# Performance work log

Measured on AMD Instinct MI355X. Metric: run time of the kernel, lower is better.

## Reference

```python
import jax, jax.numpy as jnp
import numpy as np


def setup_inputs() -> dict:
    key = jax.random.key(0)
    k1, k2, k3, k4 = jax.random.split(key, 4)
    B, C, H, W = 8, 64, 64, 64
    K = C // 8
    x = jax.random.normal(k1, (B, C, H, W), dtype=jnp.float32)
    # 1x1 conv weights (no bias): stored as [out_ch, in_ch]
    Wf = jax.random.normal(k2, (K, C), dtype=jnp.float32) * 0.05
    Wg = jax.random.normal(k3, (K, C), dtype=jnp.float32) * 0.05
    Wh = jax.random.normal(k4, (C, C), dtype=jnp.float32) * 0.05
    # gamma initialized to zero in the module; use a nonzero value so the
    # attention path contributes to the output (and gradients) in testing.
    gamma = jnp.array([0.5], dtype=jnp.float32)
    return {"x": x, "Wf": Wf, "Wg": Wg, "Wh": Wh, "gamma": gamma}


def reference(x, Wf, Wg, Wh, gamma):
    B, C, H, W = x.shape
    N = H * W
    xf = x.reshape(B, C, N)                       # [B, C, N]
    f = jnp.einsum('kc,bcn->bkn', Wf, xf)         # [B, C//8, N]
    g = jnp.einsum('kc,bcn->bkn', Wg, xf)         # [B, C//8, N]
    h = jnp.einsum('oc,bcn->bon', Wh, xf)         # [B, C, N]
    # beta[b, i, j] = f[b,:,i] . g[b,:,j]  (unscaled attention logits)
    beta = jnp.einsum('bki,bkj->bij', f, g)       # [B, N, N]
    beta = jax.nn.softmax(beta, axis=-1)
    # res[b, c, i] = sum_j h[b, c, j] * beta[b, i, j]
    res = jnp.einsum('bcj,bij->bci', h, beta)     # [B, C, N]
    res = res.reshape(B, C, H, W)
    return gamma * res + x
```

## Files before the change

kernel.cpp:

```cpp
#include <hip/hip_runtime.h>

typedef float f32x4 __attribute__((ext_vector_type(4)));
typedef float f32x16 __attribute__((ext_vector_type(16)));
typedef short s16x8 __attribute__((ext_vector_type(8)));
typedef short s16x4 __attribute__((ext_vector_type(4)));
typedef unsigned short u16;

#define NB 8
#define NC 64
#define NN 4096
#define NK 8

__device__ __forceinline__ u16 f2bf_rne(float f) {
    unsigned u = __float_as_uint(f);
    u += 0x7FFFu + ((u >> 16) & 1u);
    return (u16)(u >> 16);
}
__device__ __forceinline__ float bf2f(u16 v) {
    return __uint_as_float(((unsigned)v) << 16);
}
__device__ __forceinline__ unsigned cvt_pk_bf16(float lo, float hi) {
    unsigned r;
    asm("v_cvt_pk_bf16_f32 %0, %1, %2" : "=v"(r) : "v"(lo), "v"(hi));
    return r;
}
__device__ __forceinline__ void pl32_swap(unsigned &a, unsigned &b) {
    asm("v_permlane32_swap_b32 %0, %1" : "+v"(a), "+v"(b));
}
__device__ __forceinline__ float exp2_hw(float x) {
    return __builtin_amdgcn_exp2f(x);
}

#define Z16 ((f32x16){0.f,0.f,0.f,0.f,0.f,0.f,0.f,0.f,0.f,0.f,0.f,0.f,0.f,0.f,0.f,0.f})

__global__ __launch_bounds__(256, 4)
void precompute_qgh(const float* __restrict__ x,
                    const float* __restrict__ Wf,
                    const float* __restrict__ Wg,
                    const float* __restrict__ Wh,
                    u16* __restrict__ Qw, u16* __restrict__ Gw,
                    u16* __restrict__ Hw)
{
    const int b  = blockIdx.y;
    const int n0 = blockIdx.x * 64;
    const int t  = threadIdx.x;
    const int wave = t >> 6, lane = t & 63, col = lane & 15, quad = lane >> 4;
    const float* xb = x + (size_t)b * NC * NN;

    __shared__ __align__(16) u16 WL[80][72];
    __shared__ __align__(16) u16 XT[64][72];

    #pragma unroll
    for (int r5 = 0; r5 < 5; r5++) {
        int v = r5 * 256 + t;
        int m = v >> 4, ks = (v & 15) << 2;
        const float* src = (m < 64) ? (Wh + m * 64 + ks)
                         : (m < 72) ? (Wf + (m - 64) * 64 + ks)
                                    : (Wg + (m - 72) * 64 + ks);
        const float scl = (m >= 64 && m < 72) ? 1.44269504088896f : 1.0f;
        f32x4 wv = *(const f32x4*)src;
        *(unsigned*)&WL[m][ks]     = (unsigned)f2bf_rne(wv[0] * scl) | ((unsigned)f2bf_rne(wv[1] * scl) << 16);
        *(unsigned*)&WL[m][ks + 2] = (unsigned)f2bf_rne(wv[2] * scl) | ((unsigned)f2bf_rne(wv[3] * scl) << 16);
    }
    #pragma unroll
    for (int r4 = 0; r4 < 4; r4++) {
        int v = r4 * 256 + t;
        int c = v >> 4, ns = (v & 15) << 2;
        f32x4 xv = *(const f32x4*)(xb + (size_t)c * NN + n0 + ns);
        #pragma unroll
        for (int e = 0; e < 4; e++) XT[ns + e][c] = f2bf_rne(xv[e]);
    }
    __syncthreads();

    const int n = n0 + wave * 16 + col;
    s16x8 bfrag[2], afrag[5][2];
    #pragma unroll
    for (int s = 0; s < 2; s++)
        bfrag[s] = *(const s16x8*)&XT[wave * 16 + col][s * 32 + quad * 8];
    #pragma unroll
    for (int mt = 0; mt < 5; mt++)
        #pragma unroll
        for (int s = 0; s < 2; s++)
            afrag[mt][s] = *(const s16x8*)&WL[mt * 16 + col][s * 32 + quad * 8];

    f32x4 d[5];
    #pragma unroll
    for (int mt = 0; mt < 5; mt++) d[mt] = (f32x4){0.f, 0.f, 0.f, 0.f};
    #pragma unroll
    for (int s = 0; s < 2; s++)
        #pragma unroll
        for (int mt = 0; mt < 5; mt++)
            d[mt] = __builtin_amdgcn_mfma_f32_16x16x32_bf16(afrag[mt][s], bfrag[s], d[mt], 0, 0, 0);

    u16* Hb = Hw + (size_t)b * NC * NN;
    #pragma unroll
    for (int mt = 0; mt < 4; mt++)
        #pragma unroll
        for (int r = 0; r < 4; r++)
            Hb[(size_t)(mt * 16 + quad * 4 + r) * NN + n] = f2bf_rne(d[mt][r]);
    #pragma unroll
    for (int r = 0; r < 4; r++) {
        int m = quad * 4 + r;
        u16 v = f2bf_rne(d[4][r]);
        if (m < 8) Qw[((size_t)b * NN + n) * NK + m]       = v;
        else       Gw[((size_t)b * NN + n) * NK + (m - 8)] = v;
    }
}

__global__ __launch_bounds__(256, 2)
void attention_fused(const u16* __restrict__ Qw, const u16* __restrict__ Gw,
                     const u16* __restrict__ Hw,
                     const float* __restrict__ x, const float* __restrict__ gamma,
                     float* __restrict__ out)
{
    const int b  = blockIdx.y;
    const int i0 = blockIdx.x * 64;
    const int t  = threadIdx.x;
    const int wave = t >> 6, lane = t & 63, col = lane & 31, hi = lane >> 5;
    const int p = wave >> 1, wi = wave & 1;

    __shared__ __align__(16) u16 Vl[2][2][64][64];

    const u16* Qb = Qw + (size_t)b * NN * NK;
    const u16* Gb = Gw + (size_t)b * NN * NK;
    const u16* Hb = Hw + (size_t)b * NC * NN;

    s16x8 qf;
    #pragma unroll
    for (int q = 0; q < 8; q++) ((u16*)&qf)[q] = 0;
    if (hi == 0) qf = *(const s16x8*)(Qb + (size_t)(i0 + wi * 32 + col) * NK);

    s16x8 ones;
    #pragma unroll
    for (int q = 0; q < 8; q++) ((u16*)&ones)[q] = 0x3F80;

    f32x16 oacc[2];
    oacc[0] = Z16; oacc[1] = Z16;
    f32x16 lacc = Z16;

    const int jbase = p * 2048;
    const int tp = t & 127;
    const int vc = tp >> 3, vseg = tp & 7;
    const int swsl = (vseg ^ (vc & 7)) * 8;
    const int c7x8 = (col & 7) * 8;

    s16x8 vreg[4];
    #pragma unroll
    for (int u = 0; u < 4; u++)
        vreg[u] = *(const s16x8*)(Hb + (size_t)(vc + 16 * u) * NN + jbase + swsl);

    for (int cc = 0; cc < 32; cc++) {
        const int j0 = jbase + cc * 64;
        u16* vb = &Vl[p][cc & 1][0][0];

        s16x8 ga0, ga1;
        #pragma unroll
        for (int q = 0; q < 8; q++) { ((u16*)&ga0)[q] = 0; ((u16*)&ga1)[q] = 0; }
        if (hi == 0) {
            ga0 = *(const s16x8*)(Gb + (size_t)(j0 + col) * NK);
            ga1 = *(const s16x8*)(Gb + (size_t)(j0 + 32 + col) * NK);
        }

        #pragma unroll
        for (int u = 0; u < 4; u++)
            *(s16x8*)(vb + (vc + 16 * u) * 64 + vseg * 8) = vreg[u];
        #pragma unroll
        for (int u = 0; u < 4; u++)
            vreg[u] = *(const s16x8*)(Hb + (size_t)(vc + 16 * u) * NN + j0 + 64 + swsl);

        __syncthreads();

        #pragma unroll
        for (int jt = 0; jt < 2; jt++) {
            f32x16 S = __builtin_amdgcn_mfma_f32_32x32x16_bf16(jt ? ga1 : ga0, qf, Z16, 0, 0, 0);
            #pragma unroll
            for (int r = 0; r < 16; r++) S[r] = exp2_hw(S[r]);
            #pragma unroll
            for (int s2 = 0; s2 < 2; s2++) {
                unsigned w0 = cvt_pk_bf16(S[8*s2+0], S[8*s2+1]);
                unsigned w2 = cvt_pk_bf16(S[8*s2+4], S[8*s2+5]);
                unsigned w1 = cvt_pk_bf16(S[8*s2+2], S[8*s2+3]);
                unsigned w3 = cvt_pk_bf16(S[8*s2+6], S[8*s2+7]);
                pl32_swap(w0, w2);
                pl32_swap(w1, w3);
                union { s16x8 v; unsigned u[4]; } pb;
                pb.u[0] = w0; pb.u[1] = w1; pb.u[2] = w2; pb.u[3] = w3;
                lacc = __builtin_amdgcn_mfma_f32_32x32x16_bf16(ones, pb.v, lacc, 0, 0, 0);
                const int soff = ((jt * 4 + s2 * 2 + hi) * 8) ^ c7x8;
                s16x8 va0 = *(const s16x8*)(vb + col * 64 + soff);
                s16x8 va1 = *(const s16x8*)(vb + (32 + col) * 64 + soff);
                oacc[0] = __builtin_amdgcn_mfma_f32_32x32x16_bf16(va0, pb.v, oacc[0], 0, 0, 0);
                oacc[1] = __builtin_amdgcn_mfma_f32_32x32x16_bf16(va1, pb.v, oacc[1], 0, 0, 0);
            }
        }
    }

    float* Of = (float*)&Vl[0][0][0][0];
    float* Lf = Of + 2 * 64 * 32;
    u16*  OT  = (u16*)(Lf + 64);
    const float g = gamma[0];

    __syncthreads();
    if (p == 1) {
        #pragma unroll
        for (int ct = 0; ct < 2; ct++)
            #pragma unroll
            for (int r = 0; r < 16; r++) {
                int c = ct * 32 + (r & 3) + 8 * (r >> 2) + 4 * hi;
                Of[(wi * 64 + c) * 32 + col] = oacc[ct][r];
            }
        if (hi == 0) Lf[wi * 32 + col] = lacc[0];
    }
    __syncthreads();
    if (p == 0) {
        const float scale = g / (lacc[0] + Lf[wi * 32 + col]);
        const int i = wi * 32 + col;
        #pragma unroll
        for (int ct = 0; ct < 2; ct++)
            #pragma unroll
            for (int r = 0; r < 16; r++) {
                int c = ct * 32 + (r & 3) + 8 * (r >> 2) + 4 * hi;
                float o = (oacc[ct][r] + Of[(wi * 64 + c) * 32 + col]) * scale;
                OT[c * 64 + (((i >> 3) ^ (c & 7)) << 3) + (i & 7)] = f2bf_rne(o);
            }
    }
    __syncthreads();

    const int oc = t >> 2, q4 = t & 3;
    s16x8 v0 = *(const s16x8*)&OT[oc * 64 + (((2 * q4)     ^ (oc & 7)) << 3)];
    s16x8 v1 = *(const s16x8*)&OT[oc * 64 + (((2 * q4 + 1) ^ (oc & 7)) << 3)];
    const float* xr = x   + ((size_t)b * NC + oc) * NN + i0 + q4 * 16;
    float*      orow = out + ((size_t)b * NC + oc) * NN + i0 + q4 * 16;
    #pragma unroll
    for (int e = 0; e < 4; e++) {
        f32x4 xv = *(const f32x4*)(xr + e * 4);
        f32x4 ov;
        #pragma unroll
        for (int k = 0; k < 4; k++) {
            u16 val = (e < 2) ? (u16)((u16*)&v0)[e * 4 + k]
                              : (u16)((u16*)&v1)[(e - 2) * 4 + k];
            ov[k] = bf2f(val) + xv[k];
        }
        *(f32x4*)(orow + e * 4) = ov;
    }
}

extern "C" void kernel_launch(void* const* d_in, const int* in_sizes, int n_in,
                              void* d_out, int out_size, void* d_ws, size_t ws_size,
                              hipStream_t stream) {
    const float* x     = (const float*)d_in[0];
    const float* Wf    = (const float*)d_in[1];
    const float* Wg    = (const float*)d_in[2];
    const float* Wh    = (const float*)d_in[3];
    const float* gamma = (const float*)d_in[4];
    float* out = (float*)d_out;

    u16* Qw = (u16*)d_ws;
    u16* Gw = Qw + (size_t)NB * NN * NK;
    u16* Hw = Gw + (size_t)NB * NN * NK;

    precompute_qgh<<<dim3(64, NB), 256, 0, stream>>>(x, Wf, Wg, Wh, Qw, Gw, Hw);
    attention_fused<<<dim3(64, NB), 256, 0, stream>>>(Qw, Gw, Hw, x, gamma, out);
}
```

Before: 105.2 us.

## Restructure attention: 32-query blocks, 4-way key split, direct global V loads

Each block now handles 32 query rows instead of 64, and its four waves each take a quarter of the keys, which doubles the grid to 128x8 and raises the launch-bounds occupancy target to 4. The LDS staging of H and the per-chunk __syncthreads are removed: waves load their V fragments straight from global memory. Q and G are padded to 16 elements per position, so all lanes do the fragment loads without masking. Partial outputs and row sums are combined through a two-step LDS tree reduction, and the final residual add reads fp32 from LDS instead of a bf16 transpose buffer. The aim is to remove barrier stalls and gain parallelism, at the cost of more redundant global or L2 reads of H.

After: 138.6 us. 31.7% more time.

```diff
diff --git a/kernel.cpp b/kernel.cpp
--- a/kernel.cpp
+++ b/kernel.cpp
@@ -9,7 +9,6 @@
 #define NB 8
 #define NC 64
 #define NN 4096
-#define NK 8
 
 __device__ __forceinline__ u16 f2bf_rne(float f) {
     unsigned u = __float_as_uint(f);
@@ -98,37 +97,42 @@
         #pragma unroll
         for (int r = 0; r < 4; r++)
             Hb[(size_t)(mt * 16 + quad * 4 + r) * NN + n] = f2bf_rne(d[mt][r]);
-    #pragma unroll
-    for (int r = 0; r < 4; r++) {
-        int m = quad * 4 + r;
-        u16 v = f2bf_rne(d[4][r]);
-        if (m < 8) Qw[((size_t)b * NN + n) * NK + m]       = v;
-        else       Gw[((size_t)b * NN + n) * NK + (m - 8)] = v;
-    }
-}
-
-__global__ __launch_bounds__(256, 2)
+
+    union { s16x4 v; u16 e[4]; } pk4;
+    #pragma unroll
+    for (int r = 0; r < 4; r++) pk4.e[r] = f2bf_rne(d[4][r]);
+    u16* base = (quad < 2 ? Qw : Gw) + ((size_t)b * NN + n) * 16;
+    *(s16x4*)(base + (quad & 1) * 4) = pk4.v;
+    if ((quad & 1) == 0) {
+        s16x8 z;
+        #pragma unroll
+        for (int q = 0; q < 8; q++) ((u16*)&z)[q] = 0;
+        *(s16x8*)(base + 8) = z;
+    }
+}
+
+__global__ __launch_bounds__(256, 4)
 void attention_fused(const u16* __restrict__ Qw, const u16* __restrict__ Gw,
                      const u16* __restrict__ Hw,
                      const float* __restrict__ x, const float* __restrict__ gamma,
                      float* __restrict__ out)
 {
     const int b  = blockIdx.y;
-    const int i0 = blockIdx.x * 64;
+    const int i0 = blockIdx.x * 32;
     const int t  = threadIdx.x;
     const int wave = t >> 6, lane = t & 63, col = lane & 31, hi = lane >> 5;
-    const int p = wave >> 1, wi = wave & 1;
-
-    __shared__ __align__(16) u16 Vl[2][2][64][64];
-
-    const u16* Qb = Qw + (size_t)b * NN * NK;
-    const u16* Gb = Gw + (size_t)b * NN * NK;
+
+    __shared__ __align__(16) float R0[64][36];
+    __shared__ __align__(16) float R1[64][36];
+    __shared__ float L0[32], L1[32];
+
+    const u16* Qb = Qw + (size_t)b * NN * 16;
+    const u16* Gb = Gw + (size_t)b * NN * 16;
     const u16* Hb = Hw + (size_t)b * NC * NN;
 
-    s16x8 qf;
-    #pragma unroll
-    for (int q = 0; q < 8; q++) ((u16*)&qf)[q] = 0;
-    if (hi == 0) qf = *(const s16x8*)(Qb + (size_t)(i0 + wi * 32 + col) * NK);
+    const float g = gamma[0];
+
+    s16x8 qf = *(const s16x8*)(Qb + (size_t)(i0 + col) * 16 + hi * 8);
 
     s16x8 ones;
     #pragma unroll
@@ -138,111 +142,99 @@
     oacc[0] = Z16; oacc[1] = Z16;
     f32x16 lacc = Z16;
 
-    const int jbase = p * 2048;
-    const int tp = t & 127;
-    const int vc = tp >> 3, vseg = tp & 7;
-    const int swsl = (vseg ^ (vc & 7)) * 8;
-    const int c7x8 = (col & 7) * 8;
-
-    s16x8 vreg[4];
-    #pragma unroll
-    for (int u = 0; u < 4; u++)
-        vreg[u] = *(const s16x8*)(Hb + (size_t)(vc + 16 * u) * NN + jbase + swsl);
+    const int jbase = wave * 1024;
+
+    s16x8 ga = *(const s16x8*)(Gb + (size_t)(jbase + col) * 16 + hi * 8);
 
     for (int cc = 0; cc < 32; cc++) {
-        const int j0 = jbase + cc * 64;
-        u16* vb = &Vl[p][cc & 1][0][0];
-
-        s16x8 ga0, ga1;
-        #pragma unroll
-        for (int q = 0; q < 8; q++) { ((u16*)&ga0)[q] = 0; ((u16*)&ga1)[q] = 0; }
-        if (hi == 0) {
-            ga0 = *(const s16x8*)(Gb + (size_t)(j0 + col) * NK);
-            ga1 = *(const s16x8*)(Gb + (size_t)(j0 + 32 + col) * NK);
+        const int j0 = jbase + cc * 32;
+        const u16* hrow = Hb + (size_t)col * NN + j0 + hi * 8;
+        s16x8 va00 = *(const s16x8*)(hrow);
+        s16x8 va01 = *(const s16x8*)(hrow + 16);
+        s16x8 va10 = *(const s16x8*)(hrow + (size_t)32 * NN);
+        s16x8 va11 = *(const s16x8*)(hrow + (size_t)32 * NN + 16);
+
+        f32x16 S = __builtin_amdgcn_mfma_f32_32x32x16_bf16(ga, qf, Z16, 0, 0, 0);
+        ga = *(const s16x8*)(Gb + (size_t)(j0 + 32 + col) * 16 + hi * 8);
+
+        #pragma unroll
+        for (int r = 0; r < 16; r++) S[r] = exp2_hw(S[r]);
+
+        #pragma unroll
+        for (int s2 = 0; s2 < 2; s2++) {
+            unsigned w0 = cvt_pk_bf16(S[8*s2+0], S[8*s2+1]);
+            unsigned w2 = cvt_pk_bf16(S[8*s2+4], S[8*s2+5]);
+            unsigned w1 = cvt_pk_bf16(S[8*s2+2], S[8*s2+3]);
+            unsigned w3 = cvt_pk_bf16(S[8*s2+6], S[8*s2+7]);
+            pl32_swap(w0, w2);
+            pl32_swap(w1, w3);
+            union { s16x8 v; unsigned u[4]; } pb;
+            pb.u[0] = w0; pb.u[1] = w1; pb.u[2] = w2; pb.u[3] = w3;
+            lacc = __builtin_amdgcn_mfma_f32_32x32x16_bf16(ones, pb.v, lacc, 0, 0, 0);
+            oacc[0] = __builtin_amdgcn_mfma_f32_32x32x16_bf16(s2 ? va01 : va00, pb.v, oacc[0], 0, 0, 0);
+            oacc[1] = __builtin_amdgcn_mfma_f32_32x32x16_bf16(s2 ? va11 : va10, pb.v, oacc[1], 0, 0, 0);
         }
-
-        #pragma unroll
-        for (int u = 0; u < 4; u++)
-            *(s16x8*)(vb + (vc + 16 * u) * 64 + vseg * 8) = vreg[u];
-        #pragma unroll
-        for (int u = 0; u < 4; u++)
-            vreg[u] = *(const s16x8*)(Hb + (size_t)(vc + 16 * u) * NN + j0 + 64 + swsl);
-
-        __syncthreads();
-
-        #pragma unroll
-        for (int jt = 0; jt < 2; jt++) {
-            f32x16 S = __builtin_amdgcn_mfma_f32_32x32x16_bf16(jt ? ga1 : ga0, qf, Z16, 0, 0, 0);
-            #pragma unroll
-            for (int r = 0; r < 16; r++) S[r] = exp2_hw(S[r]);
-            #pragma unroll
-            for (int s2 = 0; s2 < 2; s2++) {
-                unsigned w0 = cvt_pk_bf16(S[8*s2+0], S[8*s2+1]);
-                unsigned w2 = cvt_pk_bf16(S[8*s2+4], S[8*s2+5]);
-                unsigned w1 = cvt_pk_bf16(S[8*s2+2], S[8*s2+3]);
-                unsigned w3 = cvt_pk_bf16(S[8*s2+6], S[8*s2+7]);
-                pl32_swap(w0, w2);
-                pl32_swap(w1, w3);
-                union { s16x8 v; unsigned u[4]; } pb;
-                pb.u[0] = w0; pb.u[1] = w1; pb.u[2] = w2; pb.u[3] = w3;
-                lacc = __builtin_amdgcn_mfma_f32_32x32x16_bf16(ones, pb.v, lacc, 0, 0, 0);
-                const int soff = ((jt * 4 + s2 * 2 + hi) * 8) ^ c7x8;
-                s16x8 va0 = *(const s16x8*)(vb + col * 64 + soff);
-                s16x8 va1 = *(const s16x8*)(vb + (32 + col) * 64 + soff);
-                oacc[0] = __builtin_amdgcn_mfma_f32_32x32x16_bf16(va0, pb.v, oacc[0], 0, 0, 0);
-                oacc[1] = __builtin_amdgcn_mfma_f32_32x32x16_bf16(va1, pb.v, oacc[1], 0, 0, 0);
-            }
-        }
-    }
-
-    float* Of = (float*)&Vl[0][0][0][0];
-    float* Lf = Of + 2 * 64 * 32;
-    u16*  OT  = (u16*)(Lf + 64);
-    const float g = gamma[0];
-
-    __syncthreads();
-    if (p == 1) {
-        #pragma unroll
-        for (int ct = 0; ct < 2; ct++)
-            #pragma unroll
-            for (int r = 0; r < 16; r++) {
-                int c = ct * 32 + (r & 3) + 8 * (r >> 2) + 4 * hi;
-                Of[(wi * 64 + c) * 32 + col] = oacc[ct][r];
-            }
-        if (hi == 0) Lf[wi * 32 + col] = lacc[0];
-    }
-    __syncthreads();
-    if (p == 0) {
-        const float scale = g / (lacc[0] + Lf[wi * 32 + col]);
-        const int i = wi * 32 + col;
-        #pragma unroll
-        for (int ct = 0; ct < 2; ct++)
-            #pragma unroll
-            for (int r = 0; r < 16; r++) {
-                int c = ct * 32 + (r & 3) + 8 * (r >> 2) + 4 * hi;
-                float o = (oacc[ct][r] + Of[(wi * 64 + c) * 32 + col]) * scale;
-                OT[c * 64 + (((i >> 3) ^ (c & 7)) << 3) + (i & 7)] = f2bf_rne(o);
+    }
+
+    if (wave & 1) {
+        float (*R)[36] = (wave == 1) ? R0 : R1;
+        float* L = (wave == 1) ? L0 : L1;
+        #pragma unroll
+        for (int ct = 0; ct < 2; ct++)
+            #pragma unroll
+            for (int r = 0; r < 16; r++) {
+                int c = ct * 32 + (r & 3) + 8 * (r >> 2) + 4 * hi;
+                R[c][col] = oacc[ct][r];
+            }
+        if (hi == 0) L[col] = lacc[0];
+    }
+    __syncthreads();
+    float lsum = lacc[0];
+    if (!(wave & 1)) {
+        float (*R)[36] = (wave == 0) ? R0 : R1;
+        float* L = (wave == 0) ? L0 : L1;
+        #pragma unroll
+        for (int ct = 0; ct < 2; ct++)
+            #pragma unroll
+            for (int r = 0; r < 16; r++) {
+                int c = ct * 32 + (r & 3) + 8 * (r >> 2) + 4 * hi;
+                oacc[ct][r] += R[c][col];
+            }
+        lsum += L[col];
+    }
+    if (wave == 2) {
+        #pragma unroll
+        for (int ct = 0; ct < 2; ct++)
+            #pragma unroll
+            for (int r = 0; r < 16; r++) {
+                int c = ct * 32 + (r & 3) + 8 * (r >> 2) + 4 * hi;
+                R1[c][col] = oacc[ct][r];
+            }
+        if (hi == 0) L1[col] = lsum;
+    }
+    __syncthreads();
+    if (wave == 0) {
+        lsum += L1[col];
+        const float scale = g / lsum;
+        #pragma unroll
+        for (int ct = 0; ct < 2; ct++)
+            #pragma unroll
+            for (int r = 0; r < 16; r++) {
+                int c = ct * 32 + (r & 3) + 8 * (r >> 2) + 4 * hi;
+                R0[c][col] = (oacc[ct][r] + R1[c][col]) * scale;
             }
     }
     __syncthreads();
 
     const int oc = t >> 2, q4 = t & 3;
-    s16x8 v0 = *(const s16x8*)&OT[oc * 64 + (((2 * q4)     ^ (oc & 7)) << 3)];
-    s16x8 v1 = *(const s16x8*)&OT[oc * 64 + (((2 * q4 + 1) ^ (oc & 7)) << 3)];
-    const float* xr = x   + ((size_t)b * NC + oc) * NN + i0 + q4 * 16;
-    float*      orow = out + ((size_t)b * NC + oc) * NN + i0 + q4 * 16;
-    #pragma unroll
-    for (int e = 0; e < 4; e++) {
-        f32x4 xv = *(const f32x4*)(xr + e * 4);
-        f32x4 ov;
-        #pragma unroll
-        for (int k = 0; k < 4; k++) {
-            u16 val = (e < 2) ? (u16)((u16*)&v0)[e * 4 + k]
-                              : (u16)((u16*)&v1)[(e - 2) * 4 + k];
-            ov[k] = bf2f(val) + xv[k];
-        }
-        *(f32x4*)(orow + e * 4) = ov;
-    }
+    const float* xr = x   + ((size_t)b * NC + oc) * NN + i0 + q4 * 8;
+    float*    orow  = out + ((size_t)b * NC + oc) * NN + i0 + q4 * 8;
+    f32x4 r0v = *(const f32x4*)&R0[oc][q4 * 8];
+    f32x4 r1v = *(const f32x4*)&R0[oc][q4 * 8 + 4];
+    f32x4 x0 = *(const f32x4*)(xr);
+    f32x4 x1 = *(const f32x4*)(xr + 4);
+    *(f32x4*)(orow)     = r0v + x0;
+    *(f32x4*)(orow + 4) = r1v + x1;
 }
 
 extern "C" void kernel_launch(void* const* d_in, const int* in_sizes, int n_in,
@@ -256,9 +248,9 @@
     float* out = (float*)d_out;
 
     u16* Qw = (u16*)d_ws;
-    u16* Gw = Qw + (size_t)NB * NN * NK;
-    u16* Hw = Gw + (size_t)NB * NN * NK;
+    u16* Gw = Qw + (size_t)NB * NN * 16;
+    u16* Hw = Gw + (size_t)NB * NN * 16;
 
     precompute_qgh<<<dim3(64, NB), 256, 0, stream>>>(x, Wf, Wg, Wh, Qw, Gw, Hw);
-    attention_fused<<<dim3(64, NB), 256, 0, stream>>>(Qw, Gw, Hw, x, gamma, out);
-}
+    attention_fused<<<dim3(128, NB), 256, 0, stream>>>(Qw, Gw, Hw, x, gamma, out);
+}
```
